# Kernel optimization log

Measured on AMD Instinct MI355X. Metric: run time of the kernel, lower is better.

The kernel has to match this reference:

```python
import jax, jax.numpy as jnp
import numpy as np
from jax import lax

SIGMA = 0.2
SPACING = 3
EPS = 1e-8

def multinomial_pool(prob, key, spacing=SPACING):
    """Stochastic multinomial max-pool over spacing x spacing blocks.
    Returns (sparse_detection [B,C,H,W], pooled_map [B,C,H/s,W/s], winner [B,C,H/s,W/s] int)."""
    B, C, H, W = prob.shape
    s = spacing
    Hb, Wb = H // s, W // s
    # [B,C,Hb,Wb,s*s]
    blocks = prob.reshape(B, C, Hb, s, Wb, s).transpose(0, 1, 2, 4, 3, 5).reshape(B, C, Hb, Wb, s * s)
    logits = jnp.log(blocks + EPS)
    g = jax.random.gumbel(key, blocks.shape, dtype=prob.dtype)
    winner = jnp.argmax(logits + g, axis=-1)                      # [B,C,Hb,Wb]
    onehot = jax.nn.one_hot(winner, s * s, dtype=prob.dtype)      # [B,C,Hb,Wb,s*s]
    sparse_blocks = blocks * onehot
    pooled = jnp.sum(sparse_blocks, axis=-1)                      # prob at winner
    sparse = sparse_blocks.reshape(B, C, Hb, Wb, s, s).transpose(0, 1, 2, 4, 3, 5).reshape(B, C, H, W)
    return sparse, pooled, winner

def crbm_layer(x, W, b, key):
    pre = lax.conv_general_dilated(x, W, window_strides=(1, 1), padding='VALID',
                                   dimension_numbers=('NCHW', 'OIHW', 'NCHW'))
    pre = (pre + b[None, :, None, None]) / (SIGMA ** 2)
    prob = jax.nn.sigmoid(pre)
    _, pooled, _ = multinomial_pool(prob, key)
    return pooled

def setup_inputs() -> dict:
    key = jax.random.key(0)
    kx, k1, k2 = jax.random.split(key, 3)
    x = jax.random.uniform(kx, (64, 3, 96, 96), dtype=jnp.float32)
    W1 = jax.random.normal(k1, (96, 3, 7, 7), dtype=jnp.float32) * 0.1
    b1 = jnp.zeros((96,), dtype=jnp.float32)
    W2 = jax.random.normal(k2, (192, 96, 7, 7), dtype=jnp.float32) * 0.1
    b2 = jnp.zeros((192,), dtype=jnp.float32)
    return {"x": x, "W1": W1, "b1": b1, "W2": W2, "b2": b2}

def reference(x, W1, b1, W2, b2):
    key = jax.random.key(42)
    kp1, kp2 = jax.random.split(key)
    h1 = crbm_layer(x, W1, b1, kp1)    # [64,96,30,30]
    h2 = crbm_layer(h1, W2, b2, kp2)   # [64,192,8,8]
    return h2
```

## Files before the change

### kernel.cpp

```cpp
#include <hip/hip_runtime.h>
#include <cstdint>
#include <math.h>


#define EPS_D 1e-8
#define INV_SIGMA2 (1.0 / (0.2 * 0.2))
#define TAU 6e-3
#define TAU1 2e-3f
#define REDO_CAP 32768
#define H1_BYTES (5529600ull * 8ull)
#define H1F32_BYTES (5529600ull * 4ull)
#define HB16_PLANE 5529600ull
#define HB16_BYTES (2ull * HB16_PLANE * 2ull)
#define CONVH_BYTES (32ull * 576ull * 192ull * 4ull)
#define WSPLIT_ELEMS (49ull * 192ull * 96ull)
#define XSPL_PLANE 2359296ull
#define XSPL_BYTES (3ull * XSPL_PLANE * 2ull)
#define W1B_BYTES (7ull * 3ull * 96ull * 32ull * 2ull)
#define RUNION_BYTES (XSPL_BYTES + W1B_BYTES)

typedef __bf16 bf16x8 __attribute__((ext_vector_type(8)));
typedef __bf16 bf16x4 __attribute__((ext_vector_type(4)));
typedef float f32x4 __attribute__((ext_vector_type(4)));

#define MFMA(A_, B_, C_) \
  __builtin_amdgcn_mfma_f32_16x16x32_bf16((A_), (B_), (C_), 0, 0, 0)

__host__ __device__ __forceinline__ void threefry2x32(
    uint32_t k0, uint32_t k1, uint32_t x0, uint32_t x1,
    uint32_t* o0, uint32_t* o1) {
  const uint32_t ks0 = k0, ks1 = k1, ks2 = k0 ^ k1 ^ 0x1BD11BDAu;
  x0 += ks0; x1 += ks1;
#define TF_R(r) { x0 += x1; x1 = (x1 << (r)) | (x1 >> (32 - (r))); x1 ^= x0; }
  TF_R(13) TF_R(15) TF_R(26) TF_R(6)
  x0 += ks1; x1 += ks2 + 1u;
  TF_R(17) TF_R(29) TF_R(16) TF_R(24)
  x0 += ks2; x1 += ks0 + 2u;
  TF_R(13) TF_R(15) TF_R(26) TF_R(6)
  x0 += ks0; x1 += ks1 + 3u;
  TF_R(17) TF_R(29) TF_R(16) TF_R(24)
  x0 += ks1; x1 += ks2 + 4u;
  TF_R(13) TF_R(15) TF_R(26) TF_R(6)
  x0 += ks2; x1 += ks0 + 5u;
#undef TF_R
  *o0 = x0; *o1 = x1;
}

__device__ __forceinline__ double fast_log(double x) {
  long long ib = __double_as_longlong(x);
  int e = (int)((ib >> 52) & 0x7ff) - 1023;
  double r = __longlong_as_double((ib & 0xfffffffffffffLL) | 0x3ff0000000000000LL);
  if (r > 1.4142135623730951) { r *= 0.5; e += 1; }
  double s = (r - 1.0) / (r + 1.0);
  double s2 = s * s;
  double t = fma(s2, fma(s2, fma(s2, fma(s2, fma(s2, fma(s2,
      1.0/15.0, 1.0/13.0), 1.0/11.0), 1.0/9.0), 1.0/7.0), 1.0/5.0), 1.0/3.0);
  double lr = fma(2.0 * s * s2, t, 2.0 * s);
  return fma((double)e, 0.6931471805599453, lr);
}

__device__ __forceinline__ double fast_exp(double x) {
  double nd = rint(x * 1.4426950408889634);
  double f = fma(nd, -0.6931471803691238, x);
  f = fma(nd, -1.9082149292705877e-10, f);
  double p = 2.505210838544172e-8;
  p = fma(p, f, 2.755731922398589e-7);
  p = fma(p, f, 2.7557319223985893e-6);
  p = fma(p, f, 2.48015873015873e-5);
  p = fma(p, f, 1.984126984126984e-4);
  p = fma(p, f, 1.3888888888888889e-3);
  p = fma(p, f, 8.333333333333333e-3);
  p = fma(p, f, 4.1666666666666664e-2);
  p = fma(p, f, 0.16666666666666666);
  p = fma(p, f, 0.5);
  p = fma(p, f, 1.0);
  p = fma(p, f, 1.0);
  return ldexp(p, (int)nd);
}

__device__ __forceinline__ double gumbel_pool9(const double (&acc)[9],
                                               double bb, uint64_t base,
                                               uint32_t kp0, uint32_t kp1) {
  double bestv = -1e308, bA = 1.0, bQ = 0.0;
#pragma unroll
  for (int k = 0; k < 9; ++k) {
    double pre = (acc[k] + bb) * INV_SIGMA2;
    double q = fast_exp(-fabs(pre));
    double A = pre >= 0.0 ? 1.0 : q;
    double opq = 1.0 + q;
    double L = fast_log(fma(EPS_D, opq, A)) - fast_log(opq);
    uint32_t o0, o1;
    uint64_t idx = base + (uint64_t)k;
    threefry2x32(kp0, kp1, (uint32_t)(idx >> 32), (uint32_t)idx, &o0, &o1);
    uint32_t bits = o0 ^ o1;
    float u = __uint_as_float((bits >> 9) | 0x3f800000u) - 1.0f;
    if (u == 0.0f) u = 1.17549435e-38f;
    float lg1 = (float)fast_log((double)u);
    double lg2 = fast_log(-(double)lg1);
    float gf = -(float)lg2;
    double v = L + (double)gf;
    if (v > bestv) { bestv = v; bA = A; bQ = q; }
  }
  return bA / (1.0 + bQ);
}

__device__ __forceinline__ double gumbel_pool9_gap(const double (&acc)[9],
                                                   double bb, uint64_t base,
                                                   uint32_t kp0, uint32_t kp1,
                                                   double* gap) {
  double bestv = -1e308, second = -1e308, bA = 1.0, bQ = 0.0;
#pragma unroll
  for (int k = 0; k < 9; ++k) {
    double pre = (acc[k] + bb) * INV_SIGMA2;
    double q = fast_exp(-fabs(pre));
    double A = pre >= 0.0 ? 1.0 : q;
    double opq = 1.0 + q;
    double L = fast_log(fma(EPS_D, opq, A)) - fast_log(opq);
    uint32_t o0, o1;
    uint64_t idx = base + (uint64_t)k;
    threefry2x32(kp0, kp1, (uint32_t)(idx >> 32), (uint32_t)idx, &o0, &o1);
    uint32_t bits = o0 ^ o1;
    float u = __uint_as_float((bits >> 9) | 0x3f800000u) - 1.0f;
    if (u == 0.0f) u = 1.17549435e-38f;
    float lg1 = (float)fast_log((double)u);
    double lg2 = fast_log(-(double)lg1);
    float gf = -(float)lg2;
    double v = L + (double)gf;
    if (v > bestv) { second = bestv; bestv = v; bA = A; bQ = q; }
    else if (v > second) second = v;
  }
  *gap = bestv - second;
  return bA / (1.0 + bQ);
}

__device__ __forceinline__ float gumbel_pool9_gap_f32(
    const float (&acc)[9], float bb, uint64_t base,
    uint32_t kp0, uint32_t kp1, float* gap) {
  float bestv = -1e30f, second = -1e30f, bA = 1.0f, bQ = 0.0f;
#pragma unroll
  for (int k = 0; k < 9; ++k) {
    float pre = (acc[k] + bb) * 25.0f;
    float q = __expf(-fabsf(pre));
    float A = pre >= 0.0f ? 1.0f : q;
    float opq = 1.0f + q;
    float L = __logf(fmaf(1e-8f, opq, A)) - __logf(opq);
    uint32_t o0, o1;
    uint64_t idx = base + (uint64_t)k;
    threefry2x32(kp0, kp1, (uint32_t)(idx >> 32), (uint32_t)idx, &o0, &o1);
    uint32_t bits = o0 ^ o1;
    float u = __uint_as_float((bits >> 9) | 0x3f800000u) - 1.0f;
    if (u == 0.0f) u = 1.17549435e-38f;
    float lg1 = __logf(u);
    float gf = -__logf(-lg1);
    float v = L + gf;
    if (v > bestv) { second = bestv; bestv = v; bA = A; bQ = q; }
    else if (v > second) second = v;
  }
  *gap = bestv - second;
  return bA / (1.0f + bQ);
}

__device__ __forceinline__ unsigned short f32_to_bf16(float v) {
  uint32_t u = __float_as_uint(v);
  return (unsigned short)((u + 0x7fffu + ((u >> 16) & 1u)) >> 16);
}
__device__ __forceinline__ float bf16_to_f32(unsigned short s) {
  return __uint_as_float(((uint32_t)s) << 16);
}

template <int LDSTRIDE, typename T>
__device__ __forceinline__ void conv_pair(const T* __restrict__ xb,
                                          const double (&w)[49],
                                          double (&a0)[9], double (&a1)[9]) {
#pragma unroll
  for (int pr = 0; pr < 12; ++pr) {
    double xr[9];
#pragma unroll
    for (int c = 0; c < 9; ++c) xr[c] = (double)xb[pr * LDSTRIDE + c];
#pragma unroll
    for (int ki = 0; ki < 3; ++ki) {
      const int u0 = pr - ki;
      if (u0 >= 0 && u0 <= 6) {
#pragma unroll
        for (int kj = 0; kj < 3; ++kj)
#pragma unroll
          for (int v = 0; v < 7; ++v)
            a0[ki * 3 + kj] = fma(xr[kj + v], w[u0 * 7 + v], a0[ki * 3 + kj]);
      }
      const int u1 = pr - 3 - ki;
      if (u1 >= 0 && u1 <= 6) {
#pragma unroll
        for (int kj = 0; kj < 3; ++kj)
#pragma unroll
          for (int v = 0; v < 7; ++v)
            a1[ki * 3 + kj] = fma(xr[kj + v], w[u1 * 7 + v], a1[ki * 3 + kj]);
      }
    }
  }
}

__global__ void init_cnt_kernel(unsigned int* __restrict__ cnt) {
  cnt[0] = 0u; cnt[1] = 0u;
}

__global__ __launch_bounds__(256, 3) void l1_kernel(
    const float* __restrict__ x, const float* __restrict__ W1,
    const float* __restrict__ b1, double* __restrict__ h1,
    float* __restrict__ h1f32, int write_f64, int write_f32,
    unsigned int* __restrict__ cnt, uint32_t kp0, uint32_t kp1) {
  const int oc   = blockIdx.x;
  const int b    = blockIdx.y;
  const int half = blockIdx.z;
  const int t = threadIdx.x;
  const int wave = t >> 6;

  if (cnt && oc == 0 && b == 0 && half == 0 && t == 0) *cnt = 0u;

  __shared__ float xs[54 * 96];

  const int p0 = 14 * half;
  const bool active = t < 240;
  const int q = t / 30, bw = t - q * 30;
  const float* xb = xs + (6 * q) * 96 + 3 * bw;

  double a0[9] = {}, a1[9] = {};
  double w[49];

#pragma unroll 1
  for (int ic = 0; ic < 3; ++ic) {
    __syncthreads();
    {
      const char* gsrc = (const char*)(x + ((size_t)b * 3 + ic) * 9216 + (3 * p0) * 96);
#pragma unroll
      for (int p = 0; p < 6; ++p) {
        int elt = p * 256 + t;
        if (elt < 1296) {
          __builtin_amdgcn_global_load_lds(
              (const __attribute__((address_space(1))) void*)(gsrc + (size_t)elt * 16),
              (__attribute__((address_space(3))) void*)((char*)xs +
                                                        (size_t)(p * 256 + wave * 64) * 16),
              16, 0, 0);
        }
      }
    }
    __syncthreads();
    {
      const float* __restrict__ wsrc = W1 + (oc * 3 + ic) * 49;
#pragma unroll
      for (int j = 0; j < 49; ++j) w[j] = (double)wsrc[j];
    }
    if (active) conv_pair<96, float>(xb, w, a0, a1);
  }

  if (active) {
    const double bb = (double)b1[oc];
    const int bh0 = p0 + 2 * q;
#pragma unroll
    for (int j = 0; j < 2; ++j) {
      const int pos = (bh0 + j) * 30 + bw;
      const uint64_t base = ((uint64_t)((b * 96 + oc) * 900 + pos)) * 9ull;
      double pooled = gumbel_pool9(j ? a1 : a0, bb, base, kp0, kp1);
      const size_t oidx = (size_t)(b * 96 + oc) * 900 + pos;
      if (write_f64) h1[oidx] = pooled;
      if (write_f32) h1f32[oidx] = (float)pooled;
    }
  }
}

__global__ __launch_bounds__(256) void x_split_kernel(
    const float* __restrict__ x, unsigned short* __restrict__ xs) {
  int idx = blockIdx.x * 256 + threadIdx.x;
  int px = idx % 96; int rest = idx / 96;
  int row = rest % 96; int b = rest / 96;
  unsigned long long pk[3] = {0ull, 0ull, 0ull};
#pragma unroll
  for (int ic = 0; ic < 3; ++ic) {
    float v = x[((size_t)(b * 3 + ic) * 96 + row) * 96 + px];
    unsigned short s0 = f32_to_bf16(v); float r1 = v - bf16_to_f32(s0);
    unsigned short s1 = f32_to_bf16(r1); float r2 = r1 - bf16_to_f32(s1);
    unsigned short s2 = f32_to_bf16(r2);
    pk[0] |= (unsigned long long)s0 << (16 * ic);
    pk[1] |= (unsigned long long)s1 << (16 * ic);
    pk[2] |= (unsigned long long)s2 << (16 * ic);
  }
#pragma unroll
  for (int p = 0; p < 3; ++p)
    *(unsigned long long*)(xs + (size_t)p * XSPL_PLANE + (size_t)idx * 4) = pk[p];
}

__global__ __launch_bounds__(256) void w1_split_kernel(
    const float* __restrict__ W1, unsigned short* __restrict__ wb) {
  int idx = blockIdx.x * 256 + threadIdx.x;
  int k = idx % 32; int rest = idx / 32;
  int oc = rest % 96; int kh = rest / 96;
  int kw = k >> 2, ic = k & 3;
  float v = (ic < 3 && kw < 7) ? W1[(((size_t)oc * 3 + ic) * 7 + kh) * 7 + kw] : 0.0f;
  unsigned short a = f32_to_bf16(v); float r1 = v - bf16_to_f32(a);
  unsigned short b = f32_to_bf16(r1); float r2 = r1 - bf16_to_f32(b);
  unsigned short c = f32_to_bf16(r2);
  wb[((size_t)(kh * 3 + 0) * 96 + oc) * 32 + k] = a;
  wb[((size_t)(kh * 3 + 1) * 96 + oc) * 32 + k] = b;
  wb[((size_t)(kh * 3 + 2) * 96 + oc) * 32 + k] = c;
}

__global__ __launch_bounds__(256) void w2_split_kernel(
    const float* __restrict__ W2, unsigned short* __restrict__ s0,
    unsigned short* __restrict__ s1, unsigned short* __restrict__ s2) {
  int idx = blockIdx.x * 256 + threadIdx.x;
  int ic = idx % 96; int rest = idx / 96;
  int oc = rest % 192; int tap = rest / 192;
  float v = W2[(size_t)(oc * 96 + ic) * 49 + tap];
  unsigned short a = f32_to_bf16(v); float r1 = v - bf16_to_f32(a);
  unsigned short b = f32_to_bf16(r1); float r2 = r1 - bf16_to_f32(b);
  unsigned short c = f32_to_bf16(r2);
  s0[idx] = a; s1[idx] = b; s2[idx] = c;
}

__global__ __launch_bounds__(256, 2) void l1_mfma_kernel(
    const unsigned short* __restrict__ xs, const unsigned short* __restrict__ wb,
    const float* __restrict__ b1, float* __restrict__ h1f32,
    unsigned short* __restrict__ hb16,
    unsigned int* __restrict__ cnt, unsigned int* __restrict__ list,
    uint32_t kp0, uint32_t kp1) {
  const int xt = blockIdx.x;
  const int yt = blockIdx.y;
  const int b  = blockIdx.z;
  const int t = threadIdx.x;
  const int w = t >> 6;
  const int l = t & 63;
  const int g = l >> 4;
  const int lr = l & 15;
  const int x0 = 30 * xt;
  const int y0 = 6 * yt;

  __shared__ __align__(16) float smem_f[17640];
  char* smem = (char*)smem_f;

  if (t < 4) smem_f[2592 + t] = 0.0f;

  {
    const int wave64 = w << 6;
#pragma unroll
    for (int p = 0; p < 3; ++p) {
      int s = p * 256 + t;
      if (s < 648) {
        int pl = s / 216;
        int r2 = s - pl * 216;
        int row = r2 / 18;
        int ch = r2 - row * 18;
        const char* src = (const char*)(xs + (size_t)pl * XSPL_PLANE +
                          ((size_t)((b * 96 + y0 + row) * 96 + x0)) * 4) + ch * 16;
        __builtin_amdgcn_global_load_lds(
            (const __attribute__((address_space(1))) void*)src,
            (__attribute__((address_space(3))) void*)(smem + (size_t)(p * 256 + wave64) * 16),
            16, 0, 0);
      }
    }
  }

  int aoff[3];
#pragma unroll
  for (int mf = 0; mf < 3; ++mf) {
    int pos = (w * 3 + mf) * 16 + lr;
    if (pos > 179) pos = 179;
    int ya = pos / 30, xxa = pos - 30 * ya;
    aoff[mf] = ya * 288 + xxa * 8 + g * 16;
  }

  f32x4 acc[3][6];
#pragma unroll
  for (int mf = 0; mf < 3; ++mf)
#pragma unroll
    for (int nf = 0; nf < 6; ++nf) acc[mf][nf] = (f32x4){0.f, 0.f, 0.f, 0.f};

  __syncthreads();

#pragma unroll 1
  for (int kh = 0; kh < 7; ++kh) {
    bf16x8 bc[6][3];
#pragma unroll
    for (int nf = 0; nf < 6; ++nf) {
      int oc = nf * 16 + lr;
#pragma unroll
      for (int pl = 0; pl < 3; ++pl)
        bc[nf][pl] = *(const bf16x8*)&wb[(((size_t)kh * 3 + pl) * 96 + oc) * 32 + 8 * g];
    }
#pragma unroll
    for (int mf = 0; mf < 3; ++mf) {
      const char* ap = smem + kh * 288 + aoff[mf];
      bf16x4 a0l = *(const bf16x4*)(ap);
      bf16x4 a0h = *(const bf16x4*)(ap + 8);
      bf16x4 a1l = *(const bf16x4*)(ap + 3456);
      bf16x4 a1h = *(const bf16x4*)(ap + 3464);
      bf16x4 a2l = *(const bf16x4*)(ap + 6912);
      bf16x4 a2h = *(const bf16x4*)(ap + 6920);
      bf16x8 a0 = __builtin_shufflevector(a0l, a0h, 0, 1, 2, 3, 4, 5, 6, 7);
      bf16x8 a1 = __builtin_shufflevector(a1l, a1h, 0, 1, 2, 3, 4, 5, 6, 7);
      bf16x8 a2 = __builtin_shufflevector(a2l, a2h, 0, 1, 2, 3, 4, 5, 6, 7);
#pragma unroll
      for (int nf = 0; nf < 6; ++nf) {
        f32x4 c = acc[mf][nf];
        c = MFMA(a0, bc[nf][0], c);
        c = MFMA(a0, bc[nf][1], c);
        c = MFMA(a1, bc[nf][0], c);
        c = MFMA(a1, bc[nf][1], c);
        c = MFMA(a0, bc[nf][2], c);
        c = MFMA(a2, bc[nf][0], c);
        acc[mf][nf] = c;
      }
    }
  }

  __syncthreads();
  {
#pragma unroll
    for (int mf = 0; mf < 3; ++mf)
#pragma unroll
      for (int nf = 0; nf < 6; ++nf)
#pragma unroll
        for (int r = 0; r < 4; ++r) {
          int pos = (w * 3 + mf) * 16 + g * 4 + r;
          if (pos < 180) smem_f[pos * 98 + nf * 16 + lr] = acc[mf][nf][r];
        }
  }
  __syncthreads();

#pragma unroll 1
  for (int i = 0; i < 8; ++i) {
    int oi = i * 256 + t;
    if (oi < 1920) {
      int oc = oi % 96; int rc = oi / 96;
      int pc = rc % 10, pr = rc / 10;
      float a[9];
      float chk = 0.0f;
#pragma unroll
      for (int dy = 0; dy < 3; ++dy)
#pragma unroll
        for (int dx = 0; dx < 3; ++dx) {
          float v = smem_f[((pr * 3 + dy) * 30 + pc * 3 + dx) * 98 + oc];
          a[dy * 3 + dx] = v;
          chk += v;
        }
      int gy = yt * 2 + pr, gx = xt * 10 + pc;
      int pos = gy * 30 + gx;
      unsigned int oidx = (unsigned int)((b * 96 + oc) * 900 + pos);
      float gap;
      float pooled = gumbel_pool9_gap_f32(a, b1[oc], (uint64_t)oidx * 9ull,
                                          kp0, kp1, &gap);
      h1f32[oidx] = pooled;
      unsigned short s0 = f32_to_bf16(pooled);
      float r1 = pooled - bf16_to_f32(s0);
      unsigned short s1 = f32_to_bf16(r1);
      size_t nidx = ((size_t)b * 900 + pos) * 96 + oc;
      hb16[nidx] = s0;
      hb16[HB16_PLANE + nidx] = s1;
      if (!(gap >= TAU1) || chk != chk) {
        unsigned int idx = atomicAdd(cnt, 1u);
        if (idx < REDO_CAP) list[idx] = oidx;
      }
    }
  }
}

__global__ __launch_bounds__(64) void l1_redo_kernel(
    const float* __restrict__ x, const float* __restrict__ W1,
    const float* __restrict__ b1, float* __restrict__ h1f32,
    unsigned short* __restrict__ hb16,
    const unsigned int* __restrict__ cnt, const unsigned int* __restrict__ list,
    uint32_t kp0, uint32_t kp1) {
  unsigned int n = *cnt;
  if (n > REDO_CAP) n = REDO_CAP;
  if (blockIdx.x >= n) return;
  const unsigned int oidx = list[blockIdx.x];
  const int gx = oidx % 30;
  const int gy = (oidx / 30) % 30;
  const int rest = oidx / 900;
  const int oc = rest % 96, b = rest / 96;
  const int lane = threadIdx.x;

  double acc[9] = {};
  if (lane < 49) {
    const int kh = lane / 7, kw = lane % 7;
#pragma unroll
    for (int ic = 0; ic < 3; ++ic) {
      double wv = (double)W1[(((size_t)oc * 3 + ic) * 7 + kh) * 7 + kw];
      const float* __restrict__ xp = x + ((size_t)(b * 3 + ic) * 96) * 96;
#pragma unroll
      for (int dy = 0; dy < 3; ++dy)
#pragma unroll
        for (int dx = 0; dx < 3; ++dx) {
          int y = 3 * gy + dy + kh, xc = 3 * gx + dx + kw;
          acc[dy * 3 + dx] = fma((double)xp[(size_t)y * 96 + xc], wv, acc[dy * 3 + dx]);
        }
    }
  }
#pragma unroll
  for (int off = 32; off; off >>= 1)
#pragma unroll
    for (int k = 0; k < 9; ++k) acc[k] += __shfl_down(acc[k], off);

  if (lane == 0) {
    double pooled = gumbel_pool9(acc, (double)b1[oc], (uint64_t)oidx * 9ull,
                                 kp0, kp1);
    float pf = (float)pooled;
    h1f32[oidx] = pf;
    unsigned short s0 = f32_to_bf16(pf);
    float r1 = pf - bf16_to_f32(s0);
    unsigned short s1 = f32_to_bf16(r1);
    size_t nidx = ((size_t)b * 900 + gy * 30 + gx) * 96 + oc;
    hb16[nidx] = s0;
    hb16[HB16_PLANE + nidx] = s1;
  }
}

__global__ __launch_bounds__(256, 3) void l2_mfma_kernel(
    const unsigned short* __restrict__ hb16,
    const unsigned short* __restrict__ wp0,
    const unsigned short* __restrict__ wp1,
    const unsigned short* __restrict__ wp2, float* __restrict__ conv,
    int b_base) {
  const int nt = blockIdx.x;
  const int my = blockIdx.y;
  const int b_local = my / 3, mt = my - 3 * b_local;
  const int b = b_base + b_local;
  const int t = threadIdx.x;
  const int l = t & 63;
  const int w = t >> 6;
  const int wm = w >> 1, wn = w & 1;
  const int g = l >> 4;
  const int lr = l & 15;
  const int wave64 = w << 6;

  __shared__ __align__(16) unsigned short As2[2 * 4 * 420 * 8];

  int rowoff[6];
#pragma unroll
  for (int mf = 0; mf < 6; ++mf) {
    int ml = wm * 96 + mf * 16 + lr;
    int yl = ml / 24, xx = ml - 24 * yl;
    rowoff[mf] = g * 6720 + (yl * 30 + xx) * 16;
  }
  const int oc0 = nt * 64 + wn * 32 + lr;

  f32x4 acc[6][2];
#pragma unroll
  for (int mf = 0; mf < 6; ++mf)
#pragma unroll
    for (int nf = 0; nf < 2; ++nf) acc[mf][nf] = (f32x4){0.f, 0.f, 0.f, 0.f};

  const size_t pixbase = ((size_t)b * 900 + 240 * (size_t)mt) * 96;

#pragma unroll 1
  for (int ch = 0; ch < 3; ++ch) {
    __syncthreads();
#pragma unroll
    for (int i = 0; i < 14; ++i) {
      int s = i * 256 + t;
      if (s < 3360) {
        int pl = s / 1680;
        int r = s - pl * 1680;
        int g2 = r / 420;
        int px = r - g2 * 420;
        const unsigned short* src = hb16 + (size_t)pl * HB16_PLANE + pixbase +
                                    (size_t)px * 96 + ch * 32 + g2 * 8;
        __builtin_amdgcn_global_load_lds(
            (const __attribute__((address_space(1))) void*)src,
            (__attribute__((address_space(3))) void*)((char*)As2 +
                                                      (size_t)(i * 256 + wave64) * 16),
            16, 0, 0);
      }
    }
    __syncthreads();

    int boff = oc0 * 96 + ch * 32 + 8 * g;
    bf16x8 bc[2][3], bn[2][3];
#pragma unroll
    for (int nf = 0; nf < 2; ++nf) {
      bc[nf][0] = *(const bf16x8*)&wp0[boff + nf * 1536];
      bc[nf][1] = *(const bf16x8*)&wp1[boff + nf * 1536];
      bc[nf][2] = *(const bf16x8*)&wp2[boff + nf * 1536];
    }
    int kh = 0, kw = 0;
#pragma unroll 1
    for (int tap = 0; tap < 49; ++tap) {
      if (tap < 48) {
        const int bo2 = boff + 18432;
#pragma unroll
        for (int nf = 0; nf < 2; ++nf) {
          bn[nf][0] = *(const bf16x8*)&wp0[bo2 + nf * 1536];
          bn[nf][1] = *(const bf16x8*)&wp1[bo2 + nf * 1536];
          bn[nf][2] = *(const bf16x8*)&wp2[bo2 + nf * 1536];
        }
        boff = bo2;
      }
      const int tapoff = (kh * 30 + kw) * 16;
#pragma unroll
      for (int mf = 0; mf < 6; ++mf) {
        const char* ap = (const char*)As2 + rowoff[mf] + tapoff;
        bf16x8 a0 = *(const bf16x8*)(ap);
        bf16x8 a1 = *(const bf16x8*)(ap + 26880);
#pragma unroll
        for (int nf = 0; nf < 2; ++nf) {
          f32x4 c = acc[mf][nf];
          c = MFMA(a0, bc[nf][0], c);
          c = MFMA(a0, bc[nf][1], c);
          c = MFMA(a1, bc[nf][0], c);
          c = MFMA(a1, bc[nf][1], c);
          c = MFMA(a0, bc[nf][2], c);
          acc[mf][nf] = c;
        }
      }
      if (tap < 48) {
#pragma unroll
        for (int nf = 0; nf < 2; ++nf)
#pragma unroll
          for (int s = 0; s < 3; ++s) bc[nf][s] = bn[nf][s];
      }
      if (++kw == 7) { kw = 0; ++kh; }
    }
  }

  const int rowsub = g * 4;
#pragma unroll
  for (int mf = 0; mf < 6; ++mf)
#pragma unroll
    for (int nf = 0; nf < 2; ++nf)
#pragma unroll
      for (int r = 0; r < 4; ++r) {
        const int m_abs = mt * 192 + wm * 96 + mf * 16 + rowsub + r;
        const int oc = oc0 + nf * 16;
        conv[((size_t)b_local * 576 + m_abs) * 192 + oc] = acc[mf][nf][r];
      }
}

__global__ __launch_bounds__(192) void l2_pool_kernel(
    const float* __restrict__ conv, const float* __restrict__ b2,
    float* __restrict__ out, unsigned int* __restrict__ cnt,
    unsigned int* __restrict__ list, uint32_t kp0, uint32_t kp1, int b_base) {
  const int pos = blockIdx.x;
  const int bl = blockIdx.y;
  const int b = b_base + bl;
  const int oc = threadIdx.x;
  const int ph = pos >> 3, pw = pos & 7;
  double a[9];
  double chk = 0.0;
  const float* __restrict__ cb = conv + (size_t)bl * 576 * 192 + oc;
#pragma unroll
  for (int dy = 0; dy < 3; ++dy)
#pragma unroll
    for (int dx = 0; dx < 3; ++dx) {
      double v = (double)cb[((size_t)((3 * ph + dy) * 24 + 3 * pw + dx)) * 192];
      a[dy * 3 + dx] = v;
      chk += v;
    }
  const unsigned int oid = (unsigned int)((b * 192 + oc) * 64 + pos);
  double gap;
  double pooled = gumbel_pool9_gap(a, (double)b2[oc], (uint64_t)oid * 9ull,
                                   kp0, kp1, &gap);
  out[oid] = (float)pooled;
  if (!(gap >= TAU) || chk != chk) {
    unsigned int idx = atomicAdd(cnt, 1u);
    if (idx < REDO_CAP) list[idx] = oid;
  }
}

__global__ __launch_bounds__(256, 3) void l2_kernel_f64(
    const double* __restrict__ h1, const float* __restrict__ W2,
    const float* __restrict__ b2, float* __restrict__ out,
    uint32_t kp0, uint32_t kp1) {
  const int octile = blockIdx.x;
  const int b      = blockIdx.y;
  const int t = threadIdx.x;
  const int wave = t >> 6;
  const int oc_local = t >> 5;
  const int li = t & 31;
  const int bw = li & 7;
  const int ph = 2 * ((li >> 3) & 1) + (li >> 4);
  const int bh0 = 2 * ph;
  const int oc = octile * 8 + oc_local;

  __shared__ double hs[2][900];
  __shared__ double wsd[2][392];

  const double* __restrict__ hb = h1 + (size_t)b * 86400;
  const float* __restrict__ wg = W2 + (size_t)octile * 8 * 4704;

  double a0[9] = {}, a1[9] = {};
  double w[49];

  auto stage = [&](int c, int buf) {
    const char* gsrc = (const char*)(hb + (size_t)c * 900);
#pragma unroll
    for (int p = 0; p < 2; ++p) {
      int elt = p * 256 + t;
      if (elt < 450) {
        __builtin_amdgcn_global_load_lds(
            (const __attribute__((address_space(1))) void*)(gsrc + (size_t)elt * 16),
            (__attribute__((address_space(3))) void*)((char*)&hs[buf][0] +
                                                      (size_t)(p * 256 + wave * 64) * 16),
            16, 0, 0);
      }
    }
#pragma unroll
    for (int p = 0; p < 2; ++p) {
      int j = p * 256 + t;
      if (j < 392) {
        int oi = j / 49, rem = j - oi * 49;
        wsd[buf][j] = (double)wg[(size_t)oi * 4704 + c * 49 + rem];
      }
    }
  };

  stage(0, 0);
#pragma unroll 1
  for (int c = 0; c < 96; ++c) {
    __syncthreads();
    if (c + 1 < 96) stage(c + 1, (c + 1) & 1);
    {
      const double* __restrict__ wsrc = &wsd[c & 1][oc_local * 49];
#pragma unroll
      for (int j = 0; j < 49; ++j) w[j] = wsrc[j];
      const double* xb = &hs[c & 1][(6 * ph) * 30 + 3 * bw];
      conv_pair<30, double>(xb, w, a0, a1);
    }
  }

  const double bb = (double)b2[oc];
#pragma unroll
  for (int j = 0; j < 2; ++j) {
    const int bh = bh0 + j;
    const uint64_t base = ((uint64_t)(((b * 192 + oc) * 8 + bh) * 8 + bw)) * 9ull;
    double pooled = gumbel_pool9(j ? a1 : a0, bb, base, kp0, kp1);
    out[(size_t)(b * 192 + oc) * 64 + bh * 8 + bw] = (float)pooled;
  }
}

__global__ __launch_bounds__(64) void l2_redo_kernel(
    const float* __restrict__ h1f, const float* __restrict__ W2,
    const float* __restrict__ b2, float* __restrict__ out,
    const unsigned int* __restrict__ cnt, const unsigned int* __restrict__ list,
    uint32_t kp0, uint32_t kp1) {
  unsigned int n = *cnt;
  if (n > REDO_CAP) n = REDO_CAP;
  if (blockIdx.x >= n) return;
  const unsigned int oid = list[blockIdx.x];
  const int sp = oid & 63, bh = sp >> 3, bw = sp & 7;
  const int rest = oid >> 6, oc = rest % 192, b = rest / 192;
  const int lane = threadIdx.x;

  double acc[9] = {};
  for (int ic = lane; ic < 96; ic += 64) {
    const float* __restrict__ xp =
        h1f + ((size_t)(b * 96 + ic) * 30 + 3 * bh) * 30 + 3 * bw;
    const float* __restrict__ wp = W2 + ((size_t)oc * 96 + ic) * 49;
    double w[49];
#pragma unroll
    for (int j = 0; j < 49; ++j) w[j] = (double)wp[j];
#pragma unroll
    for (int pr = 0; pr < 9; ++pr) {
      double xr[9];
#pragma unroll
      for (int c = 0; c < 9; ++c) xr[c] = (double)xp[pr * 30 + c];
#pragma unroll
      for (int kh = 0; kh < 3; ++kh) {
        const int u = pr - kh;
        if (u >= 0 && u <= 6) {
#pragma unroll
          for (int kw = 0; kw < 3; ++kw)
#pragma unroll
            for (int v = 0; v < 7; ++v)
              acc[kh * 3 + kw] = fma(xr[kw + v], w[u * 7 + v], acc[kh * 3 + kw]);
        }
      }
    }
  }
#pragma unroll
  for (int off = 32; off; off >>= 1)
#pragma unroll
    for (int k = 0; k < 9; ++k) acc[k] += __shfl_down(acc[k], off);

  if (lane == 0) {
    const uint64_t base = (uint64_t)oid * 9ull;
    double pooled = gumbel_pool9(acc, (double)b2[oc], base, kp0, kp1);
    out[oid] = (float)pooled;
  }
}

extern "C" void kernel_launch(void* const* d_in, const int* in_sizes, int n_in,
                              void* d_out, int out_size, void* d_ws,
                              size_t ws_size, hipStream_t stream) {
  const float* x  = (const float*)d_in[0];
  const float* W1 = (const float*)d_in[1];
  const float* b1 = (const float*)d_in[2];
  const float* W2 = (const float*)d_in[3];
  const float* b2 = (const float*)d_in[4];
  float* out = (float*)d_out;

  uint32_t kp1a, kp1b, kp2a, kp2b;
  threefry2x32(0u, 42u, 0u, 0u, &kp1a, &kp1b);
  threefry2x32(0u, 42u, 0u, 1u, &kp2a, &kp2b);

  const size_t WSPL_BYTES = WSPLIT_ELEMS * 2ull;
  const size_t need_main = H1F32_BYTES + HB16_BYTES + RUNION_BYTES +
                           3 * WSPL_BYTES + 16 + 2 * (size_t)REDO_CAP * 4;
  const size_t need_f64  = H1_BYTES;

  if (ws_size >= need_main) {
    char* wsb = (char*)d_ws;
    float* h1f32 = (float*)wsb;
    unsigned short* hb16 = (unsigned short*)(wsb + H1F32_BYTES);
    char* R = wsb + H1F32_BYTES + HB16_BYTES;
    unsigned short* xsplit = (unsigned short*)R;
    unsigned short* w1b = (unsigned short*)(R + XSPL_BYTES);
    float* conv = (float*)R;
    unsigned short* wp0 = (unsigned short*)(R + RUNION_BYTES);
    unsigned short* wp1 = wp0 + WSPLIT_ELEMS;
    unsigned short* wp2 = wp1 + WSPLIT_ELEMS;
    unsigned int* cntblk = (unsigned int*)(R + RUNION_BYTES + 3 * WSPL_BYTES);
    unsigned int* list1 = cntblk + 4;
    unsigned int* list2 = list1 + REDO_CAP;

    init_cnt_kernel<<<1, 1, 0, stream>>>(cntblk);
    x_split_kernel<<<2304, 256, 0, stream>>>(x, xsplit);
    w1_split_kernel<<<84, 256, 0, stream>>>(W1, w1b);
    w2_split_kernel<<<3528, 256, 0, stream>>>(W2, wp0, wp1, wp2);
    l1_mfma_kernel<<<dim3(3, 15, 64), 256, 0, stream>>>(
        xsplit, w1b, b1, h1f32, hb16, cntblk + 0, list1, kp1a, kp1b);
    l1_redo_kernel<<<REDO_CAP, 64, 0, stream>>>(
        x, W1, b1, h1f32, hb16, cntblk + 0, list1, kp1a, kp1b);
    l2_mfma_kernel<<<dim3(3, 96), 256, 0, stream>>>(hb16, wp0, wp1, wp2,
                                                    conv, 0);
    l2_pool_kernel<<<dim3(64, 32), 192, 0, stream>>>(conv, b2, out,
                                                     cntblk + 1, list2,
                                                     kp2a, kp2b, 0);
    l2_mfma_kernel<<<dim3(3, 96), 256, 0, stream>>>(hb16, wp0, wp1, wp2,
                                                    conv, 32);
    l2_pool_kernel<<<dim3(64, 32), 192, 0, stream>>>(conv, b2, out,
                                                     cntblk + 1, list2,
                                                     kp2a, kp2b, 32);
    l2_redo_kernel<<<REDO_CAP, 64, 0, stream>>>(h1f32, W2, b2, out,
                                                cntblk + 1, list2, kp2a, kp2b);
  } else {
    double* h1 = (double*)d_ws;
    l1_kernel<<<dim3(96, 64, 2), 256, 0, stream>>>(
        x, W1, b1, h1, (float*)0, 1, 0, (unsigned int*)0, kp1a, kp1b);
    l2_kernel_f64<<<dim3(24, 64), 256, 0, stream>>>(h1, W2, b2, out,
                                                    kp2a, kp2b);
  }
}
```

Baseline: 961.7 us.

## Halve L1 epilogue LDS, raise occupancy, and use ratio-form Gumbel argmax

```diff
diff --git a/kernel.cpp b/kernel.cpp
--- a/kernel.cpp
+++ b/kernel.cpp
@@ -7,12 +7,13 @@
 #define INV_SIGMA2 (1.0 / (0.2 * 0.2))
 #define TAU 6e-3
 #define TAU1 2e-3f
+#define RTH1 0.9980020f
+#define RTH2 0.9940180f
 #define REDO_CAP 32768
 #define H1_BYTES (5529600ull * 8ull)
 #define H1F32_BYTES (5529600ull * 4ull)
 #define HB16_PLANE 5529600ull
 #define HB16_BYTES (2ull * HB16_PLANE * 2ull)
-#define CONVH_BYTES (32ull * 576ull * 192ull * 4ull)
 #define WSPLIT_ELEMS (49ull * 192ull * 96ull)
 #define XSPL_PLANE 2359296ull
 #define XSPL_BYTES (3ull * XSPL_PLANE * 2ull)
@@ -104,59 +105,28 @@
   return bA / (1.0 + bQ);
 }
 
-__device__ __forceinline__ double gumbel_pool9_gap(const double (&acc)[9],
-                                                   double bb, uint64_t base,
-                                                   uint32_t kp0, uint32_t kp1,
-                                                   double* gap) {
-  double bestv = -1e308, second = -1e308, bA = 1.0, bQ = 0.0;
-#pragma unroll
-  for (int k = 0; k < 9; ++k) {
-    double pre = (acc[k] + bb) * INV_SIGMA2;
-    double q = fast_exp(-fabs(pre));
-    double A = pre >= 0.0 ? 1.0 : q;
-    double opq = 1.0 + q;
-    double L = fast_log(fma(EPS_D, opq, A)) - fast_log(opq);
-    uint32_t o0, o1;
-    uint64_t idx = base + (uint64_t)k;
-    threefry2x32(kp0, kp1, (uint32_t)(idx >> 32), (uint32_t)idx, &o0, &o1);
-    uint32_t bits = o0 ^ o1;
-    float u = __uint_as_float((bits >> 9) | 0x3f800000u) - 1.0f;
-    if (u == 0.0f) u = 1.17549435e-38f;
-    float lg1 = (float)fast_log((double)u);
-    double lg2 = fast_log(-(double)lg1);
-    float gf = -(float)lg2;
-    double v = L + (double)gf;
-    if (v > bestv) { second = bestv; bestv = v; bA = A; bQ = q; }
-    else if (v > second) second = v;
-  }
-  *gap = bestv - second;
-  return bA / (1.0 + bQ);
-}
-
-__device__ __forceinline__ float gumbel_pool9_gap_f32(
-    const float (&acc)[9], float bb, uint64_t base,
-    uint32_t kp0, uint32_t kp1, float* gap) {
-  float bestv = -1e30f, second = -1e30f, bA = 1.0f, bQ = 0.0f;
+__device__ __forceinline__ float gumbel_pool9_ratio(
+    const float (&acc)[9], float bb, uint32_t base,
+    uint32_t kp0, uint32_t kp1, bool* flag, float rthresh) {
+  float bestr = -1.0f, second = -1.0f, bA = 1.0f, bQ = 0.0f;
 #pragma unroll
   for (int k = 0; k < 9; ++k) {
     float pre = (acc[k] + bb) * 25.0f;
     float q = __expf(-fabsf(pre));
     float A = pre >= 0.0f ? 1.0f : q;
     float opq = 1.0f + q;
-    float L = __logf(fmaf(1e-8f, opq, A)) - __logf(opq);
+    float num = fmaf(1e-8f, opq, A);
     uint32_t o0, o1;
-    uint64_t idx = base + (uint64_t)k;
-    threefry2x32(kp0, kp1, (uint32_t)(idx >> 32), (uint32_t)idx, &o0, &o1);
+    threefry2x32(kp0, kp1, 0u, base + (uint32_t)k, &o0, &o1);
     uint32_t bits = o0 ^ o1;
     float u = __uint_as_float((bits >> 9) | 0x3f800000u) - 1.0f;
     if (u == 0.0f) u = 1.17549435e-38f;
-    float lg1 = __logf(u);
-    float gf = -__logf(-lg1);
-    float v = L + gf;
-    if (v > bestv) { second = bestv; bestv = v; bA = A; bQ = q; }
-    else if (v > second) second = v;
-  }
-  *gap = bestv - second;
+    float m = -__logf(u);
+    float r = num / (opq * m);
+    if (r > bestr) { second = bestr; bestr = r; bA = A; bQ = q; }
+    else if (r > second) second = r;
+  }
+  *flag = !(second <= bestr * rthresh);
   return bA / (1.0f + bQ);
 }
 
@@ -316,7 +286,7 @@
   s0[idx] = a; s1[idx] = b; s2[idx] = c;
 }
 
-__global__ __launch_bounds__(256, 2) void l1_mfma_kernel(
+__global__ __launch_bounds__(256, 4) void l1_mfma_kernel(
     const unsigned short* __restrict__ xs, const unsigned short* __restrict__ wb,
     const float* __restrict__ b1, float* __restrict__ h1f32,
     unsigned short* __restrict__ hb16,
@@ -333,7 +303,7 @@
   const int x0 = 30 * xt;
   const int y0 = 6 * yt;
 
-  __shared__ __align__(16) float smem_f[17640];
+  __shared__ __align__(16) float smem_f[9000];
   char* smem = (char*)smem_f;
 
   if (t < 4) smem_f[2592 + t] = 0.0f;
@@ -411,55 +381,71 @@
     }
   }
 
+  auto pool_half = [&](int ocb) {
+    int oc_l = t % 48;
+    int rc = t / 48;
+#pragma unroll 1
+    for (int i = 0; i < 4; ++i) {
+      if (i) { oc_l += 16; if (oc_l >= 48) { oc_l -= 48; rc += 6; } else rc += 5; }
+      if (rc < 20) {
+        int pc = rc < 10 ? rc : rc - 10;
+        int pr = rc < 10 ? 0 : 1;
+        float a[9];
+        float chk = 0.0f;
+#pragma unroll
+        for (int dy = 0; dy < 3; ++dy)
+#pragma unroll
+          for (int dx = 0; dx < 3; ++dx) {
+            float v = smem_f[((pr * 3 + dy) * 30 + pc * 3 + dx) * 50 + oc_l];
+            a[dy * 3 + dx] = v;
+            chk += v;
+          }
+        int oc = ocb + oc_l;
+        int gy = yt * 2 + pr, gx = xt * 10 + pc;
+        int pos = gy * 30 + gx;
+        unsigned int oidx = (unsigned int)((b * 96 + oc) * 900 + pos);
+        bool flag;
+        float pooled = gumbel_pool9_ratio(a, b1[oc], oidx * 9u,
+                                          kp0, kp1, &flag, RTH1);
+        h1f32[oidx] = pooled;
+        unsigned short s0 = f32_to_bf16(pooled);
+        float r1 = pooled - bf16_to_f32(s0);
+        unsigned short s1 = f32_to_bf16(r1);
+        size_t nidx = ((size_t)b * 900 + pos) * 96 + oc;
+        hb16[nidx] = s0;
+        hb16[HB16_PLANE + nidx] = s1;
+        if (flag || chk != chk) {
+          unsigned int idx = atomicAdd(cnt, 1u);
+          if (idx < REDO_CAP) list[idx] = oidx;
+        }
+      }
+    }
+  };
+
   __syncthreads();
-  {
-#pragma unroll
-    for (int mf = 0; mf < 3; ++mf)
-#pragma unroll
-      for (int nf = 0; nf < 6; ++nf)
-#pragma unroll
-        for (int r = 0; r < 4; ++r) {
-          int pos = (w * 3 + mf) * 16 + g * 4 + r;
-          if (pos < 180) smem_f[pos * 98 + nf * 16 + lr] = acc[mf][nf][r];
-        }
-  }
+#pragma unroll
+  for (int mf = 0; mf < 3; ++mf)
+#pragma unroll
+    for (int nf = 0; nf < 3; ++nf)
+#pragma unroll
+      for (int r = 0; r < 4; ++r) {
+        int pos = (w * 3 + mf) * 16 + g * 4 + r;
+        if (pos < 180) smem_f[pos * 50 + nf * 16 + lr] = acc[mf][nf][r];
+      }
   __syncthreads();
-
-#pragma unroll 1
-  for (int i = 0; i < 8; ++i) {
-    int oi = i * 256 + t;
-    if (oi < 1920) {
-      int oc = oi % 96; int rc = oi / 96;
-      int pc = rc % 10, pr = rc / 10;
-      float a[9];
-      float chk = 0.0f;
-#pragma unroll
-      for (int dy = 0; dy < 3; ++dy)
-#pragma unroll
-        for (int dx = 0; dx < 3; ++dx) {
-          float v = smem_f[((pr * 3 + dy) * 30 + pc * 3 + dx) * 98 + oc];
-          a[dy * 3 + dx] = v;
-          chk += v;
-        }
-      int gy = yt * 2 + pr, gx = xt * 10 + pc;
-      int pos = gy * 30 + gx;
-      unsigned int oidx = (unsigned int)((b * 96 + oc) * 900 + pos);
-      float gap;
-      float pooled = gumbel_pool9_gap_f32(a, b1[oc], (uint64_t)oidx * 9ull,
-                                          kp0, kp1, &gap);
-      h1f32[oidx] = pooled;
-      unsigned short s0 = f32_to_bf16(pooled);
-      float r1 = pooled - bf16_to_f32(s0);
-      unsigned short s1 = f32_to_bf16(r1);
-      size_t nidx = ((size_t)b * 900 + pos) * 96 + oc;
-      hb16[nidx] = s0;
-      hb16[HB16_PLANE + nidx] = s1;
-      if (!(gap >= TAU1) || chk != chk) {
-        unsigned int idx = atomicAdd(cnt, 1u);
-        if (idx < REDO_CAP) list[idx] = oidx;
-      }
-    }
-  }
+  pool_half(0);
+  __syncthreads();
+#pragma unroll
+  for (int mf = 0; mf < 3; ++mf)
+#pragma unroll
+    for (int nf = 3; nf < 6; ++nf)
+#pragma unroll
+      for (int r = 0; r < 4; ++r) {
+        int pos = (w * 3 + mf) * 16 + g * 4 + r;
+        if (pos < 180) smem_f[pos * 50 + (nf - 3) * 16 + lr] = acc[mf][nf][r];
+      }
+  __syncthreads();
+  pool_half(48);
 }
 
 __global__ __launch_bounds__(64) void l1_redo_kernel(
@@ -642,23 +628,22 @@
   const int b = b_base + bl;
   const int oc = threadIdx.x;
   const int ph = pos >> 3, pw = pos & 7;
-  double a[9];
-  double chk = 0.0;
+  float a[9];
+  float chk = 0.0f;
   const float* __restrict__ cb = conv + (size_t)bl * 576 * 192 + oc;
 #pragma unroll
   for (int dy = 0; dy < 3; ++dy)
 #pragma unroll
     for (int dx = 0; dx < 3; ++dx) {
-      double v = (double)cb[((size_t)((3 * ph + dy) * 24 + 3 * pw + dx)) * 192];
+      float v = cb[((size_t)((3 * ph + dy) * 24 + 3 * pw + dx)) * 192];
       a[dy * 3 + dx] = v;
       chk += v;
     }
   const unsigned int oid = (unsigned int)((b * 192 + oc) * 64 + pos);
-  double gap;
-  double pooled = gumbel_pool9_gap(a, (double)b2[oc], (uint64_t)oid * 9ull,
-                                   kp0, kp1, &gap);
-  out[oid] = (float)pooled;
-  if (!(gap >= TAU) || chk != chk) {
+  bool flag;
+  float pooled = gumbel_pool9_ratio(a, b2[oc], oid * 9u, kp0, kp1, &flag, RTH2);
+  out[oid] = pooled;
+  if (flag || chk != chk) {
     unsigned int idx = atomicAdd(cnt, 1u);
     if (idx < REDO_CAP) list[idx] = oid;
   }
```

After: 1.143 ms. 18.9% more time.
